# Kernel tuning notes

Measured on AMD Instinct MI355X. Metric: run time of the kernel, lower is better.

Reference implementation:

```python
import jax, jax.numpy as jnp
import numpy as np

B, C, H, W = 8, 512, 64, 64


def setup_inputs() -> dict:
    key = jax.random.key(0)
    ks = jax.random.split(key, 7)
    s = 1.0 / np.sqrt(C)  # conv2d default init scale
    return {
        "x": jax.random.normal(ks[0], (B, C, H, W), dtype=jnp.float32),
        "wq": jax.random.normal(ks[1], (C, C), dtype=jnp.float32) * s,
        "bq": jax.random.normal(ks[2], (C,), dtype=jnp.float32) * s,
        "wk": jax.random.normal(ks[3], (C, C), dtype=jnp.float32) * s,
        "bk": jax.random.normal(ks[4], (C,), dtype=jnp.float32) * s,
        "wv": jax.random.normal(ks[5], (C, C), dtype=jnp.float32) * s,
        "bv": jax.random.normal(ks[6], (C,), dtype=jnp.float32) * s,
    }


def reference(x, wq, bq, wk, bk, wv, bv):
    b, c, h, w = x.shape
    xf = x.reshape(b, c, h * w)  # (B, C, N)
    # 1x1 convs == per-pixel channel GEMMs
    q = jnp.einsum("oc,bcn->bon", wq, xf) + bq[None, :, None]
    k = jnp.einsum("oc,bcn->bon", wk, xf) + bk[None, :, None]
    v = jnp.einsum("oc,bcn->bon", wv, xf) + bv[None, :, None]
    # channel attention: (B, C, C), contraction over spatial N
    attn = jax.nn.softmax(jnp.einsum("bin,bjn->bij", q, k), axis=-1)
    out = jnp.einsum("bij,bjn->bin", attn, v)
    return out.reshape(b, c, h, w)
```

## Files before the change

kernel.cpp:

```cpp
#include <hip/hip_runtime.h>


typedef unsigned short u16;
typedef short v8s __attribute__((ext_vector_type(8)));
typedef float v4f __attribute__((ext_vector_type(4)));

#define B_ 8
#define C_ 512
#define N_ 4096

__device__ __forceinline__ u16 f2bf(float f) {
  unsigned int u = __builtin_bit_cast(unsigned int, f);
  u = u + 0x7fffu + ((u >> 16) & 1u);
  return (u16)(u >> 16);
}
__device__ __forceinline__ float bf2f(u16 h) {
  unsigned int u = ((unsigned int)h) << 16;
  return __builtin_bit_cast(float, u);
}
__device__ __forceinline__ void gld_lds16(const u16* g, u16* l) {
  __builtin_amdgcn_global_load_lds((__attribute__((address_space(1))) void*)(g),
                                   (__attribute__((address_space(3))) void*)(l),
                                   16, 0, 0);
}

template <bool SPLIT, int EPI, bool TRI>
__global__ __launch_bounds__(256) void gemm_bt(
    const u16* __restrict__ Ah, const u16* __restrict__ Al, long long sA_,
    const u16* __restrict__ Bh, const u16* __restrict__ Bl, long long sB_,
    int K, int Kc, int nsplit, int ldc,
    float* __restrict__ Cf, u16* __restrict__ Ch,
    long long sC_, const float* __restrict__ rowbias) {
  constexpr int NSH = SPLIT ? 6 : 4;
  __shared__ __attribute__((aligned(16))) u16 pool[NSH * 4096];

  int b, ks, ty_, tx_, tidx;
  if (TRI) {
    int L = (int)blockIdx.z * 10 + (int)blockIdx.x;
    int cpx = (B_ * nsplit * 10) >> 3;
    int Ls = (L & 7) * cpx + (L >> 3);
    int t = Ls % 10, z = Ls / 10;
    b = z / nsplit;
    ks = z % nsplit;
    tidx = t;
    ty_ = (t < 4) ? 0 : (t < 7) ? 1 : (t < 9) ? 2 : 3;
    tx_ = t - ((ty_ == 0) ? 0 : (ty_ == 1) ? 3 : (ty_ == 2) ? 5 : 6);
  } else {
    b = blockIdx.z / nsplit;
    ks = blockIdx.z % nsplit;
    ty_ = blockIdx.y;
    tx_ = blockIdx.x;
    tidx = ty_ * 4 + tx_;
  }
  int tid = threadIdx.x, lane = tid & 63, w = tid >> 6;
  const u16* pAh = Ah + (size_t)b * sA_ + (size_t)ty_ * 128 * K;
  const u16* pBh = Bh + (size_t)b * sB_ + (size_t)tx_ * 128 * K;
  const u16* pAl = SPLIT ? (Al + (size_t)b * sA_ + (size_t)ty_ * 128 * K) : pAh;
  const u16* pBl = SPLIT ? (Bl + (size_t)b * sB_ + (size_t)tx_ * 128 * K) : pBh;
  int wr = (w >> 1) * 64, wc = (w & 1) * 64;
  v4f acc[4][4] = {};

  int srow_off = lane >> 2;
  int gcol = ((lane & 3) ^ ((lane >> 3) & 3)) * 8;

  int kbeg = ks * Kc;
  int nIter = Kc >> 5;

  auto STAGE_HI = [&](int pb, int k0) {
    if constexpr (SPLIT) {
      u16* a = pool + pb * 4096;
      u16* bb = pool + (2 + pb) * 4096;
      for (int t2 = 0; t2 < 2; ++t2) {
        int t = w * 2 + t2;
        gld_lds16(pAh + (size_t)(t * 16 + srow_off) * K + k0 + gcol, a + t * 512);
        gld_lds16(pBh + (size_t)(t * 16 + srow_off) * K + k0 + gcol, bb + t * 512);
      }
    } else {
      u16* lds = pool + pb * 2 * 4096 + (w >> 1) * 4096;
      const u16* base = (w < 2) ? pAh : pBh;
      int o = (w & 1) * 4;
      for (int t = 0; t < 4; ++t) {
        int s = o + t;
        gld_lds16(base + (size_t)(s * 16 + srow_off) * K + k0 + gcol, lds + s * 512);
      }
    }
  };
  auto STAGE_LO = [&](int k0) {
    u16* a = pool + 4 * 4096;
    u16* bb = pool + 5 * 4096;
    for (int t2 = 0; t2 < 2; ++t2) {
      int t = w * 2 + t2;
      gld_lds16(pAl + (size_t)(t * 16 + srow_off) * K + k0 + gcol, a + t * 512);
      gld_lds16(pBl + (size_t)(t * 16 + srow_off) * K + k0 + gcol, bb + t * 512);
    }
  };

  int r = lane & 15, q = lane >> 4;
  int sw = (q ^ ((r >> 1) & 3)) * 8;

  STAGE_HI(0, kbeg);
  if constexpr (SPLIT) STAGE_LO(kbeg);
  for (int it = 0; it < nIter; ++it) {
    int cur = it & 1;
    bool pf = (it + 1 < nIter);
    if (pf) {
      STAGE_HI(cur ^ 1, kbeg + (it + 1) * 32);
      asm volatile("s_waitcnt vmcnt(4)" ::: "memory");
    } else {
      asm volatile("s_waitcnt vmcnt(0)" ::: "memory");
    }
    __builtin_amdgcn_s_barrier();
    __builtin_amdgcn_sched_barrier(0);

    const u16 *A0s, *B0s, *A1s, *B1s;
    if constexpr (SPLIT) {
      A0s = pool + cur * 4096;
      B0s = pool + (2 + cur) * 4096;
      A1s = pool + 4 * 4096;
      B1s = pool + 5 * 4096;
    } else {
      A0s = pool + cur * 2 * 4096;
      B0s = A0s + 4096;
      A1s = A0s;
      B1s = B0s;
    }
    v8s a0[4], a1[4], b0[4], b1[4];
    for (int mt = 0; mt < 4; ++mt) {
      int off = (wr + mt * 16 + r) * 32 + sw;
      a0[mt] = *(const v8s*)(const void*)(A0s + off);
      if (SPLIT) a1[mt] = *(const v8s*)(const void*)(A1s + off);
    }
    for (int nt = 0; nt < 4; ++nt) {
      int off = (wc + nt * 16 + r) * 32 + sw;
      b0[nt] = *(const v8s*)(const void*)(B0s + off);
      if (SPLIT) b1[nt] = *(const v8s*)(const void*)(B1s + off);
    }
    for (int mt = 0; mt < 4; ++mt)
      for (int nt = 0; nt < 4; ++nt) {
        acc[mt][nt] = __builtin_amdgcn_mfma_f32_16x16x32_bf16(a0[mt], b0[nt], acc[mt][nt], 0, 0, 0);
        if (SPLIT) {
          acc[mt][nt] = __builtin_amdgcn_mfma_f32_16x16x32_bf16(a0[mt], b1[nt], acc[mt][nt], 0, 0, 0);
          acc[mt][nt] = __builtin_amdgcn_mfma_f32_16x16x32_bf16(a1[mt], b0[nt], acc[mt][nt], 0, 0, 0);
        }
      }
    asm volatile("" ::: "memory");
    __builtin_amdgcn_s_barrier();
    asm volatile("" ::: "memory");
    if (SPLIT && pf) STAGE_LO(kbeg + (it + 1) * 32);
  }

  if (EPI == 4) {
    constexpr int NT = TRI ? 10 : 16;
    float* dstp = Cf + ((size_t)(b * nsplit + ks) * NT + tidx) * 16384;
    for (int mt = 0; mt < 4; ++mt)
      for (int nt = 0; nt < 4; ++nt) {
        int rl = wr + mt * 16 + q * 4;
        int cl = wc + nt * 16 + r;
        for (int e = 0; e < 4; ++e)
          dstp[(size_t)(rl + e) * 128 + cl] = acc[mt][nt][e];
      }
  } else {
    for (int mt = 0; mt < 4; ++mt)
      for (int nt = 0; nt < 4; ++nt) {
        int row0 = ty_ * 128 + wr + mt * 16 + q * 4;
        int col = tx_ * 128 + wc + nt * 16 + r;
        for (int e = 0; e < 4; ++e) {
          float vv = acc[mt][nt][e];
          size_t off = (size_t)b * sC_ + (size_t)(row0 + e) * ldc + col;
          if (EPI == 2) {
            Ch[off] = f2bf(vv);
          } else {
            Cf[off] = vv + rowbias[(size_t)b * C_ + row0 + e];
          }
        }
      }
  }
}

__global__ __launch_bounds__(256) void conv_split_g(
    const float* __restrict__ P, u16* __restrict__ h, u16* __restrict__ l) {
  __shared__ u16 th[64 * 133];
  __shared__ u16 tl[64 * 133];
  int j = blockIdx.x;
  int b = j & 7;
  int rest = j >> 3;
  int t = rest >> 1;
  int half = rest & 1;
  int rq = (t < 4) ? 0 : (t < 7) ? 1 : (t < 9) ? 2 : 3;
  int cq = t - ((rq == 0) ? 0 : (rq == 1) ? 3 : (rq == 2) ? 5 : 6);
  const float* p0 = P + ((size_t)(b * 8) * 10 + t) * 16384 + (size_t)(half * 64) * 128;
  int tid = threadIdx.x;
  int lr = tid >> 5;
  int c4 = (tid & 31) * 4;
  for (int it = 0; it < 8; ++it) {
    int row = it * 8 + lr;
    const float* pr = p0 + (size_t)row * 128 + c4;
    float v[4] = {0.f, 0.f, 0.f, 0.f};
    for (int ks = 0; ks < 8; ++ks) {
      float4 x = *(const float4*)(pr + (size_t)ks * 10 * 16384);
      v[0] += x.x; v[1] += x.y; v[2] += x.z; v[3] += x.w;
    }
    u16 h4[4], l4[4];
    for (int e = 0; e < 4; ++e) {
      h4[e] = f2bf(v[e]);
      l4[e] = f2bf(v[e] - bf2f(h4[e]));
    }
    int gr = rq * 128 + half * 64 + row, gc = cq * 128 + c4;
    size_t go = ((size_t)b << 18) + (size_t)gr * C_ + gc;
    *(ushort4*)(h + go) = make_ushort4(h4[0], h4[1], h4[2], h4[3]);
    *(ushort4*)(l + go) = make_ushort4(l4[0], l4[1], l4[2], l4[3]);
    for (int e = 0; e < 4; ++e) {
      th[row * 133 + c4 + e] = h4[e];
      tl[row * 133 + c4 + e] = l4[e];
    }
  }
  if (rq == cq) return;
  __syncthreads();
  int orw = tid >> 4;
  int oc4 = (tid & 15) * 4;
  for (int it = 0; it < 8; ++it) {
    int orr = it * 16 + orw;
    u16 h4[4], l4[4];
    for (int e = 0; e < 4; ++e) {
      h4[e] = th[(oc4 + e) * 133 + orr];
      l4[e] = tl[(oc4 + e) * 133 + orr];
    }
    int gr = cq * 128 + orr, gc = rq * 128 + half * 64 + oc4;
    size_t go = ((size_t)b << 18) + (size_t)gr * C_ + gc;
    *(ushort4*)(h + go) = make_ushort4(h4[0], h4[1], h4[2], h4[3]);
    *(ushort4*)(l + go) = make_ushort4(l4[0], l4[1], l4[2], l4[3]);
  }
}

__global__ __launch_bounds__(256) void conv_split(
    const float* __restrict__ P, u16* __restrict__ h, u16* __restrict__ l) {
  size_t i = ((size_t)blockIdx.x * 256 + threadIdx.x) * 4;
  int b = (int)(i >> 18);
  int r = (int)(i >> 9) & 511;
  int c = (int)i & 511;
  int t = (r >> 7) * 4 + (c >> 7);
  const float* p = P + ((size_t)(b * 4) * 16 + t) * 16384 +
                   (size_t)(r & 127) * 128 + (c & 127);
  float v[4] = {0.f, 0.f, 0.f, 0.f};
  for (int ks = 0; ks < 4; ++ks) {
    float4 x0 = *(const float4*)(p + (size_t)ks * 16 * 16384);
    v[0] += x0.x; v[1] += x0.y; v[2] += x0.z; v[3] += x0.w;
  }
  for (int j = 0; j < 4; ++j) {
    u16 hh = f2bf(v[j]);
    h[i + j] = hh;
    l[i + j] = f2bf(v[j] - bf2f(hh));
  }
}

__global__ __launch_bounds__(256) void split_transpose(
    const float* __restrict__ x, u16* __restrict__ xh, u16* __restrict__ xl,
    u16* __restrict__ xhT, float* __restrict__ sx16) {
  __shared__ u16 tile[64 * 66];
  int b = blockIdx.z, ct = blockIdx.y, nt = blockIdx.x;
  int tid = threadIdx.x;
  const float* xb = x + ((size_t)b * C_ + (size_t)ct * 64) * N_ + (size_t)nt * 64;
  float* sxs = sx16 + (size_t)(nt & 15) * (B_ * C_) + b * C_ + ct * 64;
  float4 v4[4];
  for (int it = 0; it < 4; ++it) {
    int idx = it * 1024 + tid * 4;
    v4[it] = *(const float4*)(xb + (size_t)(idx >> 6) * N_ + (idx & 63));
  }
  for (int it = 0; it < 4; ++it) {
    int idx = it * 1024 + tid * 4;
    int cl = idx >> 6;
    int nl = idx & 63;
    float vv[4] = {v4[it].x, v4[it].y, v4[it].z, v4[it].w};
    u16 h4[4], l4[4];
    for (int j = 0; j < 4; ++j) {
      h4[j] = f2bf(vv[j]);
      l4[j] = f2bf(vv[j] - bf2f(h4[j]));
    }
    size_t go = ((size_t)b * C_ + ct * 64 + cl) * N_ + (size_t)nt * 64 + nl;
    *(ushort4*)(xh + go) = make_ushort4(h4[0], h4[1], h4[2], h4[3]);
    *(ushort4*)(xl + go) = make_ushort4(l4[0], l4[1], l4[2], l4[3]);
    for (int j = 0; j < 4; ++j) tile[(nl + j) * 66 + cl] = h4[j];
    float s = vv[0] + vv[1] + vv[2] + vv[3];
    s += __shfl_xor(s, 1); s += __shfl_xor(s, 2);
    s += __shfl_xor(s, 4); s += __shfl_xor(s, 8);
    if ((tid & 15) == 0) atomicAdd(&sxs[cl], s);
  }
  asm volatile("s_waitcnt lgkmcnt(0)" ::: "memory");
  __builtin_amdgcn_s_barrier();
  __builtin_amdgcn_sched_barrier(0);
  for (int it = 0; it < 4; ++it) {
    int idx = it * 1024 + tid * 4;
    int nr = idx >> 6;
    int c4 = idx & 63;
    const u16* tp = tile + nr * 66 + c4;
    unsigned int lo = *(const unsigned int*)(const void*)(tp);
    unsigned int hi = *(const unsigned int*)(const void*)(tp + 2);
    size_t to = ((size_t)b * N_ + (size_t)nt * 64 + nr) * C_ + ct * 64 + c4;
    *(ushort4*)(xhT + to) = make_ushort4((u16)lo, (u16)(lo >> 16), (u16)hi, (u16)(hi >> 16));
  }
}

__global__ __launch_bounds__(256) void prep_weights(
    const float* __restrict__ wq, const float* __restrict__ wk, const float* __restrict__ wv,
    u16* __restrict__ wqh, u16* __restrict__ wql, u16* __restrict__ wkh,
    u16* __restrict__ wkl, u16* __restrict__ wvT, float* __restrict__ sx16) {
  int idx = blockIdx.x * 256 + threadIdx.x;
  if (blockIdx.x < 256) sx16[idx] = 0.0f;
  float q = wq[idx];
  u16 qh = f2bf(q);
  wqh[idx] = qh;
  wql[idx] = f2bf(q - bf2f(qh));
  float k = wk[idx];
  u16 kh = f2bf(k);
  wkh[idx] = kh;
  wkl[idx] = f2bf(k - bf2f(kh));
  float v = wv[idx];
  wvT[(size_t)(idx & 511) * C_ + (idx >> 9)] = f2bf(v);
}

__global__ __launch_bounds__(256) void bias_vec(
    const float* __restrict__ wq, const float* __restrict__ wk,
    const float* __restrict__ sx16, float* __restrict__ aq, float* __restrict__ ak) {
  int gw = blockIdx.x * 4 + (threadIdx.x >> 6);
  int lane = threadIdx.x & 63;
  int which = gw >> 12;
  int b = (gw >> 9) & 7, i = gw & 511;
  const float* wrow = (which ? wk : wq) + (size_t)i * C_;
  const float* sxb = sx16 + b * C_;
  float s = 0.f;
  for (int c = lane; c < C_; c += 64) {
    float sv = 0.f;
    for (int ss = 0; ss < 16; ++ss) sv += sxb[(size_t)ss * (B_ * C_) + c];
    s += wrow[c] * sv;
  }
  for (int o = 32; o; o >>= 1) s += __shfl_down(s, o);
  if (lane == 0) (which ? ak : aq)[b * C_ + i] = s;
}

__global__ __launch_bounds__(256) void softmax_rows(
    const float* __restrict__ P, const float* __restrict__ aq,
    const float* __restrict__ ak, const float* __restrict__ bq,
    const float* __restrict__ bk, const float* __restrict__ bv,
    u16* __restrict__ attn, float* __restrict__ obias) {
  int row = blockIdx.x * 4 + (threadIdx.x >> 6);
  int lane = threadIdx.x & 63;
  int b = row >> 9, i = row & 511;
  const float* akb = ak + b * C_;
  float aqi = aq[row], bqi = bq[i];
  float lv[8], ev[8];
  float m = -3.4e38f;
  for (int t = 0; t < 8; ++t) {
    int j = t * 64 + lane;
    int tile = (i >> 7) * 4 + (t >> 1);
    size_t base = ((size_t)(b * 4) * 16 + tile) * 16384 +
                  (size_t)(i & 127) * 128 + ((t & 1) * 64 + lane);
    float sv = 0.f;
    for (int ks = 0; ks < 4; ++ks) sv += P[base + (size_t)ks * 16 * 16384];
    float v = sv + aqi * bk[j] + bqi * (akb[j] + 4096.0f * bk[j]);
    lv[t] = v;
    m = fmaxf(m, v);
  }
  for (int o = 32; o; o >>= 1) m = fmaxf(m, __shfl_xor(m, o));
  float se = 0.f, sb = 0.f;
  for (int t = 0; t < 8; ++t) {
    int j = t * 64 + lane;
    float e = expf(lv[t] - m);
    ev[t] = e;
    se += e;
    sb += e * bv[j];
  }
  for (int o = 32; o; o >>= 1) {
    se += __shfl_xor(se, o);
    sb += __shfl_xor(sb, o);
  }
  float inv = 1.0f / se;
  for (int t = 0; t < 8; ++t) attn[(size_t)row * C_ + t * 64 + lane] = f2bf(ev[t] * inv);
  if (lane == 0) obias[row] = sb * inv;
}

extern "C" void kernel_launch(void* const* d_in, const int* in_sizes, int n_in,
                              void* d_out, int out_size, void* d_ws, size_t ws_size,
                              hipStream_t stream) {
  const float* x = (const float*)d_in[0];
  const float* wq = (const float*)d_in[1];
  const float* bq = (const float*)d_in[2];
  const float* wk = (const float*)d_in[3];
  const float* bk = (const float*)d_in[4];
  const float* wv = (const float*)d_in[5];
  const float* bv = (const float*)d_in[6];
  float* out = (float*)d_out;

  const size_t XN = (size_t)B_ * C_ * N_;
  const size_t CCt = (size_t)B_ * C_ * C_;
  const size_t W2 = (size_t)C_ * C_;
  const size_t PARTN = (size_t)B_ * 8 * 10 * 16384;

  u16* XH = (u16*)d_ws;
  u16* XL = XH + XN;
  u16* XHT = XL + XN;
  float* PART = (float*)(XHT + XN);
  u16* GH = (u16*)(PART + PARTN);
  u16* GL = GH + CCt;
  u16* UH = GL + CCt;
  u16* UL = UH + CCt;
  u16* ATTN = UL + CCt;
  u16* MH = ATTN + CCt;
  u16* WQH = MH + CCt;
  u16* WQL = WQH + W2;
  u16* WKH = WQL + W2;
  u16* WKL = WKH + W2;
  u16* WVT = WKL + W2;
  float* SX16 = (float*)(WVT + W2);
  float* AQ = SX16 + 16 * B_ * C_;
  float* AK = AQ + B_ * C_;
  float* OBIAS = AK + B_ * C_;

  prep_weights<<<W2 / 256, 256, 0, stream>>>(wq, wk, wv, WQH, WQL, WKH, WKL, WVT, SX16);
  split_transpose<<<dim3(N_ / 64, C_ / 64, B_), 256, 0, stream>>>(x, XH, XL, XHT, SX16);
  bias_vec<<<2048, 256, 0, stream>>>(wq, wk, SX16, AQ, AK);

  gemm_bt<true, 4, true><<<dim3(10, 1, B_ * 8), 256, 0, stream>>>(
      XH, XL, (long long)((size_t)C_ * N_), XH, XL, (long long)((size_t)C_ * N_),
      N_, 512, 8, C_, PART, nullptr, (long long)W2, nullptr);
  conv_split_g<<<160, 256, 0, stream>>>(PART, GH, GL);

  gemm_bt<true, 4, false><<<dim3(4, 4, B_ * 4), 256, 0, stream>>>(
      WKH, WKL, 0, GH, GL, (long long)W2, C_, 128, 4, C_, PART, nullptr,
      (long long)W2, nullptr);
  conv_split<<<CCt / 1024, 256, 0, stream>>>(PART, UH, UL);

  gemm_bt<true, 4, false><<<dim3(4, 4, B_ * 4), 256, 0, stream>>>(
      WQH, WQL, 0, UH, UL, (long long)W2, C_, 128, 4, C_, PART, nullptr,
      (long long)W2, nullptr);

  softmax_rows<<<(B_ * C_) / 4, 256, 0, stream>>>(PART, AQ, AK, bq, bk, bv, ATTN, OBIAS);

  gemm_bt<false, 2, false><<<dim3(4, 4, B_), 256, 0, stream>>>(
      ATTN, nullptr, (long long)W2, WVT, nullptr, 0, C_, 512, 1, C_, nullptr,
      MH, (long long)W2, nullptr);
  gemm_bt<false, 3, false><<<dim3(N_ / 128, 4, B_), 256, 0, stream>>>(
      MH, nullptr, (long long)W2, XHT, nullptr, (long long)((size_t)N_ * C_),
      C_, 512, 1, N_, out, nullptr, (long long)((size_t)C_ * N_), OBIAS);
}
```

Before: 280.6 us.

## Fuse fp32-to-bf16 hi/lo split into Gram GEMM loader, drop XH/XL buffers

The Gram GEMM (x·xᵀ) now reads fp32 x directly into registers and converts each tile to bf16 hi/lo pairs with v_cvt_pk_bf16_f32 before storing them in LDS. The split_transpose kernel therefore no longer writes the XH and XL arrays and only produces the transposed hi copy and the channel sums. This removes a full write and re-read of two bf16 copies of x. In exchange the GEMM loads twice as many bytes per tile, goes through registers instead of direct global-to-LDS loads, and does the conversion arithmetic inside its main loop.

```diff
diff --git a/kernel.cpp b/kernel.cpp
--- a/kernel.cpp
+++ b/kernel.cpp
@@ -24,14 +24,14 @@
                                    16, 0, 0);
 }
 
-template <bool SPLIT, int EPI, bool TRI>
+template <int MODE, int EPI, bool TRI>
 __global__ __launch_bounds__(256) void gemm_bt(
     const u16* __restrict__ Ah, const u16* __restrict__ Al, long long sA_,
     const u16* __restrict__ Bh, const u16* __restrict__ Bl, long long sB_,
     int K, int Kc, int nsplit, int ldc,
     float* __restrict__ Cf, u16* __restrict__ Ch,
     long long sC_, const float* __restrict__ rowbias) {
-  constexpr int NSH = SPLIT ? 6 : 4;
+  constexpr int NSH = (MODE == 1) ? 6 : 4;
   __shared__ __attribute__((aligned(16))) u16 pool[NSH * 4096];
 
   int b, ks, ty_, tx_, tidx;
@@ -53,100 +53,189 @@
     tidx = ty_ * 4 + tx_;
   }
   int tid = threadIdx.x, lane = tid & 63, w = tid >> 6;
-  const u16* pAh = Ah + (size_t)b * sA_ + (size_t)ty_ * 128 * K;
-  const u16* pBh = Bh + (size_t)b * sB_ + (size_t)tx_ * 128 * K;
-  const u16* pAl = SPLIT ? (Al + (size_t)b * sA_ + (size_t)ty_ * 128 * K) : pAh;
-  const u16* pBl = SPLIT ? (Bl + (size_t)b * sB_ + (size_t)tx_ * 128 * K) : pBh;
   int wr = (w >> 1) * 64, wc = (w & 1) * 64;
   v4f acc[4][4] = {};
 
   int srow_off = lane >> 2;
   int gcol = ((lane & 3) ^ ((lane >> 3) & 3)) * 8;
-
+  int r = lane & 15, q = lane >> 4;
+  int sw = (q ^ ((r >> 1) & 3)) * 8;
   int kbeg = ks * Kc;
   int nIter = Kc >> 5;
 
-  auto STAGE_HI = [&](int pb, int k0) {
-    if constexpr (SPLIT) {
-      u16* a = pool + pb * 4096;
-      u16* bb = pool + (2 + pb) * 4096;
-      for (int t2 = 0; t2 < 2; ++t2) {
-        int t = w * 2 + t2;
-        gld_lds16(pAh + (size_t)(t * 16 + srow_off) * K + k0 + gcol, a + t * 512);
-        gld_lds16(pBh + (size_t)(t * 16 + srow_off) * K + k0 + gcol, bb + t * 512);
-      }
-    } else {
-      u16* lds = pool + pb * 2 * 4096 + (w >> 1) * 4096;
-      const u16* base = (w < 2) ? pAh : pBh;
-      int o = (w & 1) * 4;
-      for (int t = 0; t < 4; ++t) {
-        int s = o + t;
-        gld_lds16(base + (size_t)(s * 16 + srow_off) * K + k0 + gcol, lds + s * 512);
-      }
-    }
-  };
-  auto STAGE_LO = [&](int k0) {
-    u16* a = pool + 4 * 4096;
-    u16* bb = pool + 5 * 4096;
-    for (int t2 = 0; t2 < 2; ++t2) {
-      int t = w * 2 + t2;
-      gld_lds16(pAl + (size_t)(t * 16 + srow_off) * K + k0 + gcol, a + t * 512);
-      gld_lds16(pBl + (size_t)(t * 16 + srow_off) * K + k0 + gcol, bb + t * 512);
-    }
-  };
-
-  int r = lane & 15, q = lane >> 4;
-  int sw = (q ^ ((r >> 1) & 3)) * 8;
-
-  STAGE_HI(0, kbeg);
-  if constexpr (SPLIT) STAGE_LO(kbeg);
-  for (int it = 0; it < nIter; ++it) {
-    int cur = it & 1;
-    bool pf = (it + 1 < nIter);
-    if (pf) {
-      STAGE_HI(cur ^ 1, kbeg + (it + 1) * 32);
-      asm volatile("s_waitcnt vmcnt(4)" ::: "memory");
-    } else {
-      asm volatile("s_waitcnt vmcnt(0)" ::: "memory");
-    }
-    __builtin_amdgcn_s_barrier();
-    __builtin_amdgcn_sched_barrier(0);
-
-    const u16 *A0s, *B0s, *A1s, *B1s;
-    if constexpr (SPLIT) {
-      A0s = pool + cur * 4096;
-      B0s = pool + (2 + cur) * 4096;
-      A1s = pool + 4 * 4096;
-      B1s = pool + 5 * 4096;
-    } else {
-      A0s = pool + cur * 2 * 4096;
-      B0s = A0s + 4096;
-      A1s = A0s;
-      B1s = B0s;
-    }
-    v8s a0[4], a1[4], b0[4], b1[4];
-    for (int mt = 0; mt < 4; ++mt) {
-      int off = (wr + mt * 16 + r) * 32 + sw;
-      a0[mt] = *(const v8s*)(const void*)(A0s + off);
-      if (SPLIT) a1[mt] = *(const v8s*)(const void*)(A1s + off);
-    }
-    for (int nt = 0; nt < 4; ++nt) {
-      int off = (wc + nt * 16 + r) * 32 + sw;
-      b0[nt] = *(const v8s*)(const void*)(B0s + off);
-      if (SPLIT) b1[nt] = *(const v8s*)(const void*)(B1s + off);
-    }
-    for (int mt = 0; mt < 4; ++mt)
+  if constexpr (MODE == 2) {
+    const float* fA = (const float*)(const void*)Ah + (size_t)b * sA_ +
+                      (size_t)ty_ * 128 * K;
+    const float* fB = (const float*)(const void*)Bh + (size_t)b * sB_ +
+                      (size_t)tx_ * 128 * K;
+    const float* gb0 = ((w < 2) ? fA : fB) +
+                       (size_t)((w & 1) * 64 + (lane >> 3)) * K + (lane & 7) * 4;
+    u16* hb = pool + ((w < 2) ? 0 : 2) * 4096;
+    u16* lb = hb + 4096;
+
+    auto LOADF = [&](float4* rr, int k0) {
+#pragma unroll
+      for (int t = 0; t < 8; ++t)
+        rr[t] = *(const float4*)(gb0 + k0 + (size_t)(t * 8) * K);
+    };
+    auto STOREF = [&](float4* rr) {
+#pragma unroll
+      for (int t = 0; t < 8; ++t) {
+        int row = (w & 1) * 64 + t * 8 + (lane >> 3);
+        int s = ((lane & 7) >> 1) ^ ((row >> 1) & 3);
+        int off = row * 32 + s * 8 + ((lane & 7) & 1) * 4;
+        float4 v = rr[t];
+        unsigned int ph0, ph1, pl0, pl1;
+        asm("v_cvt_pk_bf16_f32 %0, %1, %2" : "=v"(ph0) : "v"(v.x), "v"(v.y));
+        asm("v_cvt_pk_bf16_f32 %0, %1, %2" : "=v"(ph1) : "v"(v.z), "v"(v.w));
+        float h0 = __builtin_bit_cast(float, ph0 << 16);
+        float h1 = __builtin_bit_cast(float, ph0 & 0xffff0000u);
+        float h2 = __builtin_bit_cast(float, ph1 << 16);
+        float h3 = __builtin_bit_cast(float, ph1 & 0xffff0000u);
+        asm("v_cvt_pk_bf16_f32 %0, %1, %2" : "=v"(pl0) : "v"(v.x - h0), "v"(v.y - h1));
+        asm("v_cvt_pk_bf16_f32 %0, %1, %2" : "=v"(pl1) : "v"(v.z - h2), "v"(v.w - h3));
+        *(uint2*)(void*)(hb + off) = make_uint2(ph0, ph1);
+        *(uint2*)(void*)(lb + off) = make_uint2(pl0, pl1);
+      }
+    };
+    auto STEP = [&]() {
+      const u16* A0s = pool;
+      const u16* A1s = pool + 4096;
+      const u16* B0s = pool + 2 * 4096;
+      const u16* B1s = pool + 3 * 4096;
+      v8s a0[4], a1[4], b0[4], b1[4];
+#pragma unroll
+      for (int mt = 0; mt < 4; ++mt) {
+        int off = (wr + mt * 16 + r) * 32 + sw;
+        a0[mt] = *(const v8s*)(const void*)(A0s + off);
+        a1[mt] = *(const v8s*)(const void*)(A1s + off);
+      }
+#pragma unroll
       for (int nt = 0; nt < 4; ++nt) {
-        acc[mt][nt] = __builtin_amdgcn_mfma_f32_16x16x32_bf16(a0[mt], b0[nt], acc[mt][nt], 0, 0, 0);
-        if (SPLIT) {
+        int off = (wc + nt * 16 + r) * 32 + sw;
+        b0[nt] = *(const v8s*)(const void*)(B0s + off);
+        b1[nt] = *(const v8s*)(const void*)(B1s + off);
+      }
+#pragma unroll
+      for (int mt = 0; mt < 4; ++mt)
+#pragma unroll
+        for (int nt = 0; nt < 4; ++nt) {
+          acc[mt][nt] = __builtin_amdgcn_mfma_f32_16x16x32_bf16(a0[mt], b0[nt], acc[mt][nt], 0, 0, 0);
           acc[mt][nt] = __builtin_amdgcn_mfma_f32_16x16x32_bf16(a0[mt], b1[nt], acc[mt][nt], 0, 0, 0);
           acc[mt][nt] = __builtin_amdgcn_mfma_f32_16x16x32_bf16(a1[mt], b0[nt], acc[mt][nt], 0, 0, 0);
         }
-      }
-    asm volatile("" ::: "memory");
-    __builtin_amdgcn_s_barrier();
-    asm volatile("" ::: "memory");
-    if (SPLIT && pf) STAGE_LO(kbeg + (it + 1) * 32);
+    };
+
+    float4 r0[8], r1[8];
+    LOADF(r0, kbeg);
+    for (int it = 0; it < nIter; it += 2) {
+      if (it + 1 < nIter) LOADF(r1, kbeg + (it + 1) * 32);
+      STOREF(r0);
+      asm volatile("s_waitcnt lgkmcnt(0)" ::: "memory");
+      __builtin_amdgcn_s_barrier();
+      __builtin_amdgcn_sched_barrier(0);
+      STEP();
+      asm volatile("" ::: "memory");
+      __builtin_amdgcn_s_barrier();
+      asm volatile("" ::: "memory");
+      if (it + 1 < nIter) {
+        if (it + 2 < nIter) LOADF(r0, kbeg + (it + 2) * 32);
+        STOREF(r1);
+        asm volatile("s_waitcnt lgkmcnt(0)" ::: "memory");
+        __builtin_amdgcn_s_barrier();
+        __builtin_amdgcn_sched_barrier(0);
+        STEP();
+        asm volatile("" ::: "memory");
+        __builtin_amdgcn_s_barrier();
+        asm volatile("" ::: "memory");
+      }
+    }
+  } else {
+    constexpr bool SPLIT = (MODE == 1);
+    const u16* pAh = Ah + (size_t)b * sA_ + (size_t)ty_ * 128 * K;
+    const u16* pBh = Bh + (size_t)b * sB_ + (size_t)tx_ * 128 * K;
+    const u16* pAl = SPLIT ? (Al + (size_t)b * sA_ + (size_t)ty_ * 128 * K) : pAh;
+    const u16* pBl = SPLIT ? (Bl + (size_t)b * sB_ + (size_t)tx_ * 128 * K) : pBh;
+
+    auto STAGE_HI = [&](int pb, int k0) {
+      if constexpr (SPLIT) {
+        u16* a = pool + pb * 4096;
+        u16* bb = pool + (2 + pb) * 4096;
+        for (int t2 = 0; t2 < 2; ++t2) {
+          int t = w * 2 + t2;
+          gld_lds16(pAh + (size_t)(t * 16 + srow_off) * K + k0 + gcol, a + t * 512);
+          gld_lds16(pBh + (size_t)(t * 16 + srow_off) * K + k0 + gcol, bb + t * 512);
+        }
+      } else {
+        u16* lds = pool + pb * 2 * 4096 + (w >> 1) * 4096;
+        const u16* base = (w < 2) ? pAh : pBh;
+        int o = (w & 1) * 4;
+        for (int t = 0; t < 4; ++t) {
+          int s = o + t;
+          gld_lds16(base + (size_t)(s * 16 + srow_off) * K + k0 + gcol, lds + s * 512);
+        }
+      }
+    };
+    auto STAGE_LO = [&](int k0) {
+      u16* a = pool + 4 * 4096;
+      u16* bb = pool + 5 * 4096;
+      for (int t2 = 0; t2 < 2; ++t2) {
+        int t = w * 2 + t2;
+        gld_lds16(pAl + (size_t)(t * 16 + srow_off) * K + k0 + gcol, a + t * 512);
+        gld_lds16(pBl + (size_t)(t * 16 + srow_off) * K + k0 + gcol, bb + t * 512);
+      }
+    };
+
+    STAGE_HI(0, kbeg);
+    if constexpr (SPLIT) STAGE_LO(kbeg);
+    for (int it = 0; it < nIter; ++it) {
+      int cur = it & 1;
+      bool pf = (it + 1 < nIter);
+      if (pf) {
+        STAGE_HI(cur ^ 1, kbeg + (it + 1) * 32);
+        asm volatile("s_waitcnt vmcnt(4)" ::: "memory");
+      } else {
+        asm volatile("s_waitcnt vmcnt(0)" ::: "memory");
+      }
+      __builtin_amdgcn_s_barrier();
+      __builtin_amdgcn_sched_barrier(0);
+
+      const u16 *A0s, *B0s, *A1s, *B1s;
+      if constexpr (SPLIT) {
+        A0s = pool + cur * 4096;
+        B0s = pool + (2 + cur) * 4096;
+        A1s = pool + 4 * 4096;
+        B1s = pool + 5 * 4096;
+      } else {
+        A0s = pool + cur * 2 * 4096;
+        B0s = A0s + 4096;
+        A1s = A0s;
+        B1s = B0s;
+      }
+      v8s a0[4], a1[4], b0[4], b1[4];
+      for (int mt = 0; mt < 4; ++mt) {
+        int off = (wr + mt * 16 + r) * 32 + sw;
+        a0[mt] = *(const v8s*)(const void*)(A0s + off);
+        if (SPLIT) a1[mt] = *(const v8s*)(const void*)(A1s + off);
+      }
+      for (int nt = 0; nt < 4; ++nt) {
+        int off = (wc + nt * 16 + r) * 32 + sw;
+        b0[nt] = *(const v8s*)(const void*)(B0s + off);
+        if (SPLIT) b1[nt] = *(const v8s*)(const void*)(B1s + off);
+      }
+      for (int mt = 0; mt < 4; ++mt)
+        for (int nt = 0; nt < 4; ++nt) {
+          acc[mt][nt] = __builtin_amdgcn_mfma_f32_16x16x32_bf16(a0[mt], b0[nt], acc[mt][nt], 0, 0, 0);
+          if (SPLIT) {
+            acc[mt][nt] = __builtin_amdgcn_mfma_f32_16x16x32_bf16(a0[mt], b1[nt], acc[mt][nt], 0, 0, 0);
+            acc[mt][nt] = __builtin_amdgcn_mfma_f32_16x16x32_bf16(a1[mt], b0[nt], acc[mt][nt], 0, 0, 0);
+          }
+        }
+      asm volatile("" ::: "memory");
+      __builtin_amdgcn_s_barrier();
+      asm volatile("" ::: "memory");
+      if (SPLIT && pf) STAGE_LO(kbeg + (it + 1) * 32);
+    }
   }
 
   if (EPI == 4) {
@@ -254,8 +343,7 @@
 }
 
 __global__ __launch_bounds__(256) void split_transpose(
-    const float* __restrict__ x, u16* __restrict__ xh, u16* __restrict__ xl,
-    u16* __restrict__ xhT, float* __restrict__ sx16) {
+    const float* __restrict__ x, u16* __restrict__ xhT, float* __restrict__ sx16) {
   __shared__ u16 tile[64 * 66];
   int b = blockIdx.z, ct = blockIdx.y, nt = blockIdx.x;
   int tid = threadIdx.x;
@@ -271,15 +359,7 @@
     int cl = idx >> 6;
     int nl = idx & 63;
     float vv[4] = {v4[it].x, v4[it].y, v4[it].z, v4[it].w};
-    u16 h4[4], l4[4];
-    for (int j = 0; j < 4; ++j) {
-      h4[j] = f2bf(vv[j]);
-      l4[j] = f2bf(vv[j] - bf2f(h4[j]));
-    }
-    size_t go = ((size_t)b * C_ + ct * 64 + cl) * N_ + (size_t)nt * 64 + nl;
-    *(ushort4*)(xh + go) = make_ushort4(h4[0], h4[1], h4[2], h4[3]);
-    *(ushort4*)(xl + go) = make_ushort4(l4[0], l4[1], l4[2], l4[3]);
-    for (int j = 0; j < 4; ++j) tile[(nl + j) * 66 + cl] = h4[j];
+    for (int j = 0; j < 4; ++j) tile[(nl + j) * 66 + cl] = f2bf(vv[j]);
     float s = vv[0] + vv[1] + vv[2] + vv[3];
     s += __shfl_xor(s, 1); s += __shfl_xor(s, 2);
     s += __shfl_xor(s, 4); s += __shfl_xor(s, 8);
@@ -395,9 +475,7 @@
   const size_t W2 = (size_t)C_ * C_;
   const size_t PARTN = (size_t)B_ * 8 * 10 * 16384;
 
-  u16* XH = (u16*)d_ws;
-  u16* XL = XH + XN;
-  u16* XHT = XL + XN;
+  u16* XHT = (u16*)d_ws;
   float* PART = (float*)(XHT + XN);
   u16* GH = (u16*)(PART + PARTN);
   u16* GL = GH + CCt;
@@ -416,29 +494,30 @@
   float* OBIAS = AK + B_ * C_;
 
   prep_weights<<<W2 / 256, 256, 0, stream>>>(wq, wk, wv, WQH, WQL, WKH, WKL, WVT, SX16);
-  split_transpose<<<dim3(N_ / 64, C_ / 64, B_), 256, 0, stream>>>(x, XH, XL, XHT, SX16);
+  split_transpose<<<dim3(N_ / 64, C_ / 64, B_), 256, 0, stream>>>(x, XHT, SX16);
   bias_vec<<<2048, 256, 0, stream>>>(wq, wk, SX16, AQ, AK);
 
-  gemm_bt<true, 4, true><<<dim3(10, 1, B_ * 8), 256, 0, stream>>>(
-      XH, XL, (long long)((size_t)C_ * N_), XH, XL, (long long)((size_t)C_ * N_),
+  gemm_bt<2, 4, true><<<dim3(10, 1, B_ * 8), 256, 0, stream>>>(
+      (const u16*)x, nullptr, (long long)((size_t)C_ * N_),
+      (const u16*)x, nullptr, (long long)((size_t)C_ * N_),
       N_, 512, 8, C_, PART, nullptr, (long long)W2, nullptr);
   conv_split_g<<<160, 256, 0, stream>>>(PART, GH, GL);
 
-  gemm_bt<true, 4, false><<<dim3(4, 4, B_ * 4), 256, 0, stream>>>(
+  gemm_bt<1, 4, false><<<dim3(4, 4, B_ * 4), 256, 0, stream>>>(
       WKH, WKL, 0, GH, GL, (long long)W2, C_, 128, 4, C_, PART, nullptr,
       (long long)W2, nullptr);
   conv_split<<<CCt / 1024, 256, 0, stream>>>(PART, UH, UL);
 
-  gemm_bt<true, 4, false><<<dim3(4, 4, B_ * 4), 256, 0, stream>>>(
+  gemm_bt<1, 4, false><<<dim3(4, 4, B_ * 4), 256, 0, stream>>>(
       WQH, WQL, 0, UH, UL, (long long)W2, C_, 128, 4, C_, PART, nullptr,
       (long long)W2, nullptr);
 
   softmax_rows<<<(B_ * C_) / 4, 256, 0, stream>>>(PART, AQ, AK, bq, bk, bv, ATTN, OBIAS);
 
-  gemm_bt<false, 2, false><<<dim3(4, 4, B_), 256, 0, stream>>>(
+  gemm_bt<0, 2, false><<<dim3(4, 4, B_), 256, 0, stream>>>(
       ATTN, nullptr, (long long)W2, WVT, nullptr, 0, C_, 512, 1, C_, nullptr,
       MH, (long long)W2, nullptr);
-  gemm_bt<false, 3, false><<<dim3(N_ / 128, 4, B_), 256, 0, stream>>>(
+  gemm_bt<0, 3, false><<<dim3(N_ / 128, 4, B_), 256, 0, stream>>>(
       MH, nullptr, (long long)W2, XHT, nullptr, (long long)((size_t)N_ * C_),
       C_, 512, 1, N_, out, nullptr, (long long)((size_t)C_ * N_), OBIAS);
 }
```

After: 284.9 us. No clear change (+1.6%).
